# Performance work log

Measured on AMD Instinct MI355X. Metric: run time of the kernel, lower is better.

The kernel has to match this reference:

```python
import jax, jax.numpy as jnp
import numpy as np

B = 262144
I = 128   # input_len
H = 128   # h_len (must equal c_len structurally)
C = 128   # c_len
O = 128   # output_len
STD = 0.05  # keras random_normal default stddev


def setup_inputs() -> dict:
    key = jax.random.key(0)
    ks = jax.random.split(key, 14)
    inp = {
        "c_": jax.random.normal(ks[0], (B, C), dtype=jnp.float32),
        "h_": jax.random.normal(ks[1], (B, H), dtype=jnp.float32),
        "x": jax.random.normal(ks[2], (B, I), dtype=jnp.float32),
        # gate weights [C, I+H] and biases [C]
        "w": jax.random.normal(ks[3], (C, I + H), dtype=jnp.float32) * STD,
        "wi": jax.random.normal(ks[4], (C, I + H), dtype=jnp.float32) * STD,
        "wf": jax.random.normal(ks[5], (C, I + H), dtype=jnp.float32) * STD,
        "wo": jax.random.normal(ks[6], (C, I + H), dtype=jnp.float32) * STD,
        "w_out": jax.random.normal(ks[7], (O, H), dtype=jnp.float32) * STD,
        "b": jax.random.normal(ks[8], (C,), dtype=jnp.float32) * STD,
        "bi": jax.random.normal(ks[9], (C,), dtype=jnp.float32) * STD,
        "bf": jax.random.normal(ks[10], (C,), dtype=jnp.float32) * STD,
        "bo": jax.random.normal(ks[11], (C,), dtype=jnp.float32) * STD,
        "b_out": jax.random.normal(ks[12], (O,), dtype=jnp.float32) * STD,
    }
    return inp


def reference(c_, h_, x, w, wi, wf, wo, w_out, b, bi, bf, bo, b_out):
    # [B, I+H]
    xh = jnp.concatenate([x, h_], axis=-1)
    # Fuse the 4 gate matmuls into one GEMM with stacked weights [4C, I+H]
    W = jnp.concatenate([w, wi, wf, wo], axis=0)
    Bv = jnp.concatenate([b, bi, bf, bo], axis=0)
    gates = xh @ W.T + Bv                      # [B, 4C]
    gz, gi, gf, go = jnp.split(gates, 4, axis=-1)
    z = jnp.tanh(gz)
    zi = jax.nn.sigmoid(gi)
    zf = jax.nn.sigmoid(gf)
    zo = jax.nn.sigmoid(go)
    c = zf * c_ + zi * z                       # [B, C]
    h = zo * jnp.tanh(c)                       # [B, C] (== H)
    y = jax.nn.sigmoid(h @ w_out.T + b_out)    # [B, O]
    return (c, h, y)
```

## Files before the change

kernel.cpp:

```cpp
#include <hip/hip_runtime.h>

#define TB 262144

typedef short bf16x8 __attribute__((ext_vector_type(8)));
typedef float f32x16 __attribute__((ext_vector_type(16)));

__device__ __forceinline__ unsigned short f2bf(float f) {
  unsigned int u = __float_as_uint(f);
  unsigned int r = (u + 0x7fffu + ((u >> 16) & 1u)) >> 16;
  return (unsigned short)r;
}
__device__ __forceinline__ float sigmoid_f(float x) {
  return __builtin_amdgcn_rcpf(1.f + __expf(-x));
}
__device__ __forceinline__ float tanh_f(float x) {
  return 1.f - 2.f * __builtin_amdgcn_rcpf(__expf(2.f * x) + 1.f);
}

__global__ void wconv_kernel(const float* __restrict__ w, const float* __restrict__ wi,
                             const float* __restrict__ wf, const float* __restrict__ wo,
                             const float* __restrict__ wout, unsigned short* __restrict__ dst) {
  int i = blockIdx.x * 256 + threadIdx.x;
  float v;
  if (i < 32768) v = w[i];
  else if (i < 65536) v = wi[i - 32768];
  else if (i < 98304) v = wf[i - 65536];
  else if (i < 131072) v = wo[i - 98304];
  else v = wout[i - 131072];
  dst[i] = f2bf(v);
}

__global__ __launch_bounds__(256, 3) void lstm_main(
    const float* __restrict__ c_prev, const float* __restrict__ h_prev,
    const float* __restrict__ x, const unsigned short* __restrict__ wbf,
    const float* __restrict__ b, const float* __restrict__ bi,
    const float* __restrict__ bf_, const float* __restrict__ bo,
    const float* __restrict__ b_out,
    float* __restrict__ out_c, float* __restrict__ out_h, float* __restrict__ out_y) {
  __shared__ unsigned short us_xh[8192];
  __shared__ unsigned short us_h[4096];

  const int tid = threadIdx.x;
  const int wave = tid >> 6;
  const int lane = tid & 63;
  const int l31 = lane & 31;
  const int lhi = lane >> 5;
  const int kb_lane = lhi * 8;
  const int row0 = blockIdx.x * 32;
  const int j0 = wave * 32;
  const int jcol = j0 + l31;

  {
#pragma unroll
    for (int it = 0; it < 4; ++it) {
      const int cid = it * 256 + tid;
      const int r = cid >> 5;
      const int c4 = (cid & 31) * 4;
      const float4 vx = *reinterpret_cast<const float4*>(&x[(size_t)(row0 + r) * 128 + c4]);
      ushort4 ux; ux.x = f2bf(vx.x); ux.y = f2bf(vx.y); ux.z = f2bf(vx.z); ux.w = f2bf(vx.w);
      *reinterpret_cast<ushort4*>(&us_xh[(r * 256 + c4) ^ ((r & 7) << 3)]) = ux;
    }
#pragma unroll
    for (int it = 0; it < 4; ++it) {
      const int cid = it * 256 + tid;
      const int r = cid >> 5;
      const int c4 = (cid & 31) * 4;
      const float4 vh = *reinterpret_cast<const float4*>(&h_prev[(size_t)(row0 + r) * 128 + c4]);
      ushort4 uh; uh.x = f2bf(vh.x); uh.y = f2bf(vh.y); uh.z = f2bf(vh.z); uh.w = f2bf(vh.w);
      *reinterpret_cast<ushort4*>(&us_xh[(r * 256 + 128 + c4) ^ ((r & 7) << 3)]) = uh;
    }
  }
  __syncthreads();

  float cpre[16];
#pragma unroll
  for (int reg = 0; reg < 16; ++reg) {
    const int r = (reg & 3) + 8 * (reg >> 2) + 4 * lhi;
    cpre[reg] = c_prev[(size_t)(row0 + r) * 128 + jcol];
  }

  f32x16 accz = {}, acci = {}, accf = {}, acco = {};
#pragma unroll
  for (int kk = 0; kk < 16; ++kk) {
    const int kb = kk * 16 + kb_lane;
    const bf16x8 a8 =
        *reinterpret_cast<const bf16x8*>(&us_xh[(l31 * 256 + kb) ^ ((l31 & 7) << 3)]);
    const int woff = jcol * 256 + kb;
    const bf16x8 bz8 = *reinterpret_cast<const bf16x8*>(&wbf[woff]);
    const bf16x8 bi8 = *reinterpret_cast<const bf16x8*>(&wbf[32768 + woff]);
    const bf16x8 bf8 = *reinterpret_cast<const bf16x8*>(&wbf[65536 + woff]);
    const bf16x8 bo8 = *reinterpret_cast<const bf16x8*>(&wbf[98304 + woff]);
    accz = __builtin_amdgcn_mfma_f32_32x32x16_bf16(a8, bz8, accz, 0, 0, 0);
    acci = __builtin_amdgcn_mfma_f32_32x32x16_bf16(a8, bi8, acci, 0, 0, 0);
    accf = __builtin_amdgcn_mfma_f32_32x32x16_bf16(a8, bf8, accf, 0, 0, 0);
    acco = __builtin_amdgcn_mfma_f32_32x32x16_bf16(a8, bo8, acco, 0, 0, 0);
  }

  const float bz_s = b[jcol];
  const float bi_s = bi[jcol];
  const float bf_s = bf_[jcol];
  const float bo_s = bo[jcol];
#pragma unroll
  for (int reg = 0; reg < 16; ++reg) {
    const int r = (reg & 3) + 8 * (reg >> 2) + 4 * lhi;
    const size_t gi = (size_t)(row0 + r) * 128 + jcol;
    const float z  = tanh_f(accz[reg] + bz_s);
    const float zi = sigmoid_f(acci[reg] + bi_s);
    const float zf = sigmoid_f(accf[reg] + bf_s);
    const float zo = sigmoid_f(acco[reg] + bo_s);
    const float cvv = zf * cpre[reg] + zi * z;
    const float hvv = zo * tanh_f(cvv);
    out_c[gi] = cvv;
    out_h[gi] = hvv;
    us_h[(r * 128 + jcol) ^ ((r & 7) << 3)] = f2bf(hvv);
  }
  __syncthreads();

  f32x16 accy = {};
#pragma unroll
  for (int ks = 0; ks < 8; ++ks) {
    const int kb = ks * 16 + kb_lane;
    const bf16x8 a8 =
        *reinterpret_cast<const bf16x8*>(&us_h[(l31 * 128 + kb) ^ ((l31 & 7) << 3)]);
    const bf16x8 bw =
        *reinterpret_cast<const bf16x8*>(&wbf[131072 + jcol * 128 + kb]);
    accy = __builtin_amdgcn_mfma_f32_32x32x16_bf16(a8, bw, accy, 0, 0, 0);
  }
  const float by_s = b_out[jcol];
#pragma unroll
  for (int reg = 0; reg < 16; ++reg) {
    const int r = (reg & 3) + 8 * (reg >> 2) + 4 * lhi;
    out_y[(size_t)(row0 + r) * 128 + jcol] = sigmoid_f(accy[reg] + by_s);
  }
}

extern "C" void kernel_launch(void* const* d_in, const int* in_sizes, int n_in,
                              void* d_out, int out_size, void* d_ws, size_t ws_size,
                              hipStream_t stream) {
  const float* c_    = (const float*)d_in[0];
  const float* h_    = (const float*)d_in[1];
  const float* x     = (const float*)d_in[2];
  const float* w     = (const float*)d_in[3];
  const float* wi    = (const float*)d_in[4];
  const float* wf    = (const float*)d_in[5];
  const float* wo    = (const float*)d_in[6];
  const float* wout  = (const float*)d_in[7];
  const float* b     = (const float*)d_in[8];
  const float* bi    = (const float*)d_in[9];
  const float* bf_   = (const float*)d_in[10];
  const float* bo    = (const float*)d_in[11];
  const float* b_out = (const float*)d_in[12];

  unsigned short* wbf = (unsigned short*)d_ws;
  float* out_c = (float*)d_out;
  float* out_h = out_c + (size_t)TB * 128;
  float* out_y = out_h + (size_t)TB * 128;

  hipLaunchKernelGGL(wconv_kernel, dim3(576), dim3(256), 0, stream,
                     w, wi, wf, wo, wout, wbf);
  hipLaunchKernelGGL(lstm_main, dim3(8192), dim3(256), 0, stream,
                     c_, h_, x, wbf, b, bi, bf_, bo, b_out, out_c, out_h, out_y);
}
```

Baseline: 390.9 us.

## Process four row tiles per block with register-prefetched x/h pipeline

```diff
diff --git a/kernel.cpp b/kernel.cpp
--- a/kernel.cpp
+++ b/kernel.cpp
@@ -30,7 +30,7 @@
   dst[i] = f2bf(v);
 }
 
-__global__ __launch_bounds__(256, 3) void lstm_main(
+__global__ __launch_bounds__(256, 2) void lstm_main(
     const float* __restrict__ c_prev, const float* __restrict__ h_prev,
     const float* __restrict__ x, const unsigned short* __restrict__ wbf,
     const float* __restrict__ b, const float* __restrict__ bi,
@@ -46,92 +46,124 @@
   const int l31 = lane & 31;
   const int lhi = lane >> 5;
   const int kb_lane = lhi * 8;
-  const int row0 = blockIdx.x * 32;
   const int j0 = wave * 32;
   const int jcol = j0 + l31;
+  const int base_row = blockIdx.x * 128;
 
-  {
-#pragma unroll
-    for (int it = 0; it < 4; ++it) {
-      const int cid = it * 256 + tid;
-      const int r = cid >> 5;
-      const int c4 = (cid & 31) * 4;
-      const float4 vx = *reinterpret_cast<const float4*>(&x[(size_t)(row0 + r) * 128 + c4]);
-      ushort4 ux; ux.x = f2bf(vx.x); ux.y = f2bf(vx.y); ux.z = f2bf(vx.z); ux.w = f2bf(vx.w);
-      *reinterpret_cast<ushort4*>(&us_xh[(r * 256 + c4) ^ ((r & 7) << 3)]) = ux;
-    }
-#pragma unroll
-    for (int it = 0; it < 4; ++it) {
-      const int cid = it * 256 + tid;
-      const int r = cid >> 5;
-      const int c4 = (cid & 31) * 4;
-      const float4 vh = *reinterpret_cast<const float4*>(&h_prev[(size_t)(row0 + r) * 128 + c4]);
-      ushort4 uh; uh.x = f2bf(vh.x); uh.y = f2bf(vh.y); uh.z = f2bf(vh.z); uh.w = f2bf(vh.w);
-      *reinterpret_cast<ushort4*>(&us_xh[(r * 256 + 128 + c4) ^ ((r & 7) << 3)]) = uh;
-    }
+  float4 sx[2][4], sh[2][4];
+
+#define ISSUE_XH(P, ROW0)                                                        \
+  {                                                                              \
+    _Pragma("unroll") for (int it = 0; it < 4; ++it) {                           \
+      const int cid = it * 256 + tid;                                            \
+      const int r = cid >> 5;                                                    \
+      const int c4 = (cid & 31) * 4;                                             \
+      sx[P][it] = *reinterpret_cast<const float4*>(&x[(size_t)((ROW0) + r) * 128 + c4]); \
+      sh[P][it] = *reinterpret_cast<const float4*>(&h_prev[(size_t)((ROW0) + r) * 128 + c4]); \
+    }                                                                            \
   }
+
+#define WRITE_LDS(P)                                                             \
+  {                                                                              \
+    _Pragma("unroll") for (int it = 0; it < 4; ++it) {                           \
+      const int cid = it * 256 + tid;                                            \
+      const int r = cid >> 5;                                                    \
+      const int c4 = (cid & 31) * 4;                                             \
+      const int sw = (r & 7) << 3;                                               \
+      ushort4 ux;                                                                \
+      ux.x = f2bf(sx[P][it].x); ux.y = f2bf(sx[P][it].y);                        \
+      ux.z = f2bf(sx[P][it].z); ux.w = f2bf(sx[P][it].w);                        \
+      ushort4 uh;                                                                \
+      uh.x = f2bf(sh[P][it].x); uh.y = f2bf(sh[P][it].y);                        \
+      uh.z = f2bf(sh[P][it].z); uh.w = f2bf(sh[P][it].w);                        \
+      *reinterpret_cast<ushort4*>(&us_xh[(r * 256 + c4) ^ sw]) = ux;             \
+      *reinterpret_cast<ushort4*>(&us_xh[(r * 256 + 128 + c4) ^ sw]) = uh;       \
+    }                                                                            \
+  }
+
+  ISSUE_XH(0, base_row)
+  WRITE_LDS(0)
+  ISSUE_XH(1, base_row + 32)
   __syncthreads();
 
-  float cpre[16];
 #pragma unroll
-  for (int reg = 0; reg < 16; ++reg) {
-    const int r = (reg & 3) + 8 * (reg >> 2) + 4 * lhi;
-    cpre[reg] = c_prev[(size_t)(row0 + r) * 128 + jcol];
+  for (int t = 0; t < 4; ++t) {
+    const int row0 = base_row + t * 32;
+
+    float cpre[16];
+#pragma unroll
+    for (int reg = 0; reg < 16; ++reg) {
+      const int r = (reg & 3) + 8 * (reg >> 2) + 4 * lhi;
+      cpre[reg] = c_prev[(size_t)(row0 + r) * 128 + jcol];
+    }
+
+    f32x16 accz = {}, acci = {}, accf = {}, acco = {};
+#pragma unroll
+    for (int kk = 0; kk < 16; ++kk) {
+      const int kb = kk * 16 + kb_lane;
+      const bf16x8 a8 =
+          *reinterpret_cast<const bf16x8*>(&us_xh[(l31 * 256 + kb) ^ ((l31 & 7) << 3)]);
+      const int woff = jcol * 256 + kb;
+      const bf16x8 bz8 = *reinterpret_cast<const bf16x8*>(&wbf[woff]);
+      const bf16x8 bi8 = *reinterpret_cast<const bf16x8*>(&wbf[32768 + woff]);
+      const bf16x8 bf8 = *reinterpret_cast<const bf16x8*>(&wbf[65536 + woff]);
+      const bf16x8 bo8 = *reinterpret_cast<const bf16x8*>(&wbf[98304 + woff]);
+      accz = __builtin_amdgcn_mfma_f32_32x32x16_bf16(a8, bz8, accz, 0, 0, 0);
+      acci = __builtin_amdgcn_mfma_f32_32x32x16_bf16(a8, bi8, acci, 0, 0, 0);
+      accf = __builtin_amdgcn_mfma_f32_32x32x16_bf16(a8, bf8, accf, 0, 0, 0);
+      acco = __builtin_amdgcn_mfma_f32_32x32x16_bf16(a8, bo8, acco, 0, 0, 0);
+    }
+
+    const float bz_s = b[jcol];
+    const float bi_s = bi[jcol];
+    const float bf_s = bf_[jcol];
+    const float bo_s = bo[jcol];
+#pragma unroll
+    for (int reg = 0; reg < 16; ++reg) {
+      const int r = (reg & 3) + 8 * (reg >> 2) + 4 * lhi;
+      const size_t gi = (size_t)(row0 + r) * 128 + jcol;
+      const float z  = tanh_f(accz[reg] + bz_s);
+      const float zi = sigmoid_f(acci[reg] + bi_s);
+      const float zf = sigmoid_f(accf[reg] + bf_s);
+      const float zo = sigmoid_f(acco[reg] + bo_s);
+      const float cvv = zf * cpre[reg] + zi * z;
+      const float hvv = zo * tanh_f(cvv);
+      out_c[gi] = cvv;
+      out_h[gi] = hvv;
+      us_h[(r * 128 + jcol) ^ ((r & 7) << 3)] = f2bf(hvv);
+    }
+    __syncthreads();
+
+    if (t < 3) {
+      if ((t + 1) & 1) { WRITE_LDS(1) } else { WRITE_LDS(0) }
+    }
+
+    f32x16 accy = {};
+#pragma unroll
+    for (int ks = 0; ks < 8; ++ks) {
+      const int kb = ks * 16 + kb_lane;
+      const bf16x8 a8 =
+          *reinterpret_cast<const bf16x8*>(&us_h[(l31 * 128 + kb) ^ ((l31 & 7) << 3)]);
+      const bf16x8 bw =
+          *reinterpret_cast<const bf16x8*>(&wbf[131072 + jcol * 128 + kb]);
+      accy = __builtin_amdgcn_mfma_f32_32x32x16_bf16(a8, bw, accy, 0, 0, 0);
+    }
+    const float by_s = b_out[jcol];
+#pragma unroll
+    for (int reg = 0; reg < 16; ++reg) {
+      const int r = (reg & 3) + 8 * (reg >> 2) + 4 * lhi;
+      out_y[(size_t)(row0 + r) * 128 + jcol] = sigmoid_f(accy[reg] + by_s);
+    }
+
+    if (t < 2) {
+      if (t & 1) { ISSUE_XH(1, base_row + (t + 2) * 32) }
+      else       { ISSUE_XH(0, base_row + (t + 2) * 32) }
+    }
+
+    if (t < 3) __syncthreads();
   }
-
-  f32x16 accz = {}, acci = {}, accf = {}, acco = {};
-#pragma unroll
-  for (int kk = 0; kk < 16; ++kk) {
-    const int kb = kk * 16 + kb_lane;
-    const bf16x8 a8 =
-        *reinterpret_cast<const bf16x8*>(&us_xh[(l31 * 256 + kb) ^ ((l31 & 7) << 3)]);
-    const int woff = jcol * 256 + kb;
-    const bf16x8 bz8 = *reinterpret_cast<const bf16x8*>(&wbf[woff]);
-    const bf16x8 bi8 = *reinterpret_cast<const bf16x8*>(&wbf[32768 + woff]);
-    const bf16x8 bf8 = *reinterpret_cast<const bf16x8*>(&wbf[65536 + woff]);
-    const bf16x8 bo8 = *reinterpret_cast<const bf16x8*>(&wbf[98304 + woff]);
-    accz = __builtin_amdgcn_mfma_f32_32x32x16_bf16(a8, bz8, accz, 0, 0, 0);
-    acci = __builtin_amdgcn_mfma_f32_32x32x16_bf16(a8, bi8, acci, 0, 0, 0);
-    accf = __builtin_amdgcn_mfma_f32_32x32x16_bf16(a8, bf8, accf, 0, 0, 0);
-    acco = __builtin_amdgcn_mfma_f32_32x32x16_bf16(a8, bo8, acco, 0, 0, 0);
-  }
-
-  const float bz_s = b[jcol];
-  const float bi_s = bi[jcol];
-  const float bf_s = bf_[jcol];
-  const float bo_s = bo[jcol];
-#pragma unroll
-  for (int reg = 0; reg < 16; ++reg) {
-    const int r = (reg & 3) + 8 * (reg >> 2) + 4 * lhi;
-    const size_t gi = (size_t)(row0 + r) * 128 + jcol;
-    const float z  = tanh_f(accz[reg] + bz_s);
-    const float zi = sigmoid_f(acci[reg] + bi_s);
-    const float zf = sigmoid_f(accf[reg] + bf_s);
-    const float zo = sigmoid_f(acco[reg] + bo_s);
-    const float cvv = zf * cpre[reg] + zi * z;
-    const float hvv = zo * tanh_f(cvv);
-    out_c[gi] = cvv;
-    out_h[gi] = hvv;
-    us_h[(r * 128 + jcol) ^ ((r & 7) << 3)] = f2bf(hvv);
-  }
-  __syncthreads();
-
-  f32x16 accy = {};
-#pragma unroll
-  for (int ks = 0; ks < 8; ++ks) {
-    const int kb = ks * 16 + kb_lane;
-    const bf16x8 a8 =
-        *reinterpret_cast<const bf16x8*>(&us_h[(l31 * 128 + kb) ^ ((l31 & 7) << 3)]);
-    const bf16x8 bw =
-        *reinterpret_cast<const bf16x8*>(&wbf[131072 + jcol * 128 + kb]);
-    accy = __builtin_amdgcn_mfma_f32_32x32x16_bf16(a8, bw, accy, 0, 0, 0);
-  }
-  const float by_s = b_out[jcol];
-#pragma unroll
-  for (int reg = 0; reg < 16; ++reg) {
-    const int r = (reg & 3) + 8 * (reg >> 2) + 4 * lhi;
-    out_y[(size_t)(row0 + r) * 128 + jcol] = sigmoid_f(accy[reg] + by_s);
-  }
+#undef ISSUE_XH
+#undef WRITE_LDS
 }
 
 extern "C" void kernel_launch(void* const* d_in, const int* in_sizes, int n_in,
@@ -158,6 +190,6 @@
 
   hipLaunchKernelGGL(wconv_kernel, dim3(576), dim3(256), 0, stream,
                      w, wi, wf, wo, wout, wbf);
-  hipLaunchKernelGGL(lstm_main, dim3(8192), dim3(256), 0, stream,
+  hipLaunchKernelGGL(lstm_main, dim3(2048), dim3(256), 0, stream,
                      c_, h_, x, wbf, b, bi, bf_, bo, b_out, out_c, out_h, out_y);
 }
```

New measurement: 383.9 us. Within noise of the previous version (-1.8%).
